# Optimization experiments

Hardware: AMD Instinct MI355X
Metric: run time of the kernel (lower is better)

## Reference

```python
import jax, jax.numpy as jnp
import numpy as np

NUM_POINTS = 4_000_000
RADIUS = 2.5
IMG = 1024


def setup_inputs() -> dict:
    key = jax.random.key(0)
    k1, k2, k3, k4 = jax.random.split(key, 4)
    # Uniform sampling inside a sphere, mirroring the torch __init__
    phi = jax.random.uniform(k1, (NUM_POINTS,)) * 2 * np.pi
    costheta = jax.random.uniform(k2, (NUM_POINTS,)) * 2 - 1
    u = jax.random.uniform(k3, (NUM_POINTS,))
    theta = jnp.arccos(costheta)
    r = RADIUS * u ** (1.0 / 3.0)
    x = r * jnp.sin(theta) * jnp.cos(phi)
    y = r * jnp.sin(theta) * jnp.sin(phi)
    z = r * jnp.cos(theta)
    positions = jnp.stack([x, y, z], axis=-1).astype(jnp.float32)  # [N,3]
    colors = jax.random.uniform(k4, (NUM_POINTS, 3), dtype=jnp.float32)
    # Camera at origin looking down +z, points translated to z in [2.5, 7.5]
    camera_pose = jnp.eye(4, dtype=jnp.float32).at[2, 3].set(5.0)
    intrinsics = jnp.array([[800.0, 0.0, 512.0],
                            [0.0, 800.0, 512.0],
                            [0.0, 0.0, 1.0]], dtype=jnp.float32)
    return {"positions": positions, "colors": colors,
            "camera_pose": camera_pose, "intrinsics": intrinsics,
            "H": IMG, "W": IMG}


def reference(positions, colors, camera_pose, intrinsics, H, W):
    # points_cam = (R @ P^T)^T + t^T
    R = camera_pose[:3, :3]
    t = camera_pose[:3, 3]
    pc = positions @ R.T + t  # [N,3]
    x, y, z = pc[:, 0], pc[:, 1], pc[:, 2]
    fx, fy = intrinsics[0, 0], intrinsics[1, 1]
    cx, cy = intrinsics[0, 2], intrinsics[1, 2]
    u = fx * x / z + cx
    v = fy * y / z + cy
    # int() truncation toward zero, matching the torch loop
    xi = u.astype(jnp.int32)
    yi = v.astype(jnp.int32)
    valid = (xi >= 0) & (xi < W) & (yi >= 0) & (yi < H)
    n = positions.shape[0]
    pix = jnp.where(valid, yi * W + xi, H * W)  # invalid -> sentinel segment
    winner = jax.ops.segment_max(jnp.arange(n, dtype=jnp.int32), pix,
                                 num_segments=H * W + 1)[: H * W]
    has = winner >= 0  # empty segments get iinfo(int32).min
    img_flat = jnp.where(has[:, None],
                         colors[jnp.clip(winner, 0, n - 1)],
                         jnp.float32(0.0))  # [H*W, 3]
    img = img_flat.reshape(H, W, 3).transpose(2, 0, 1)[None]  # [1,3,H,W]
    return jnp.clip(img, 0.0, 1.0)
```

## Files before the change

kernel.cpp:

```cpp
#include <hip/hip_runtime.h>


#define NB      1024
#define TB      512
#define NT      1024
#define PPB_MAX 4096
#define IMGW    1024
#define IMGHW   (1024 * 1024)

__host__ __device__ __forceinline__ unsigned align8u(unsigned x) {
    return (x + 7u) & ~7u;
}

__global__ void __launch_bounds__(TB)
binsort_kernel(const float* __restrict__ pos,
               const float* __restrict__ pose,
               const float* __restrict__ intr,
               unsigned* __restrict__ bins,
               unsigned* __restrict__ histG,
               int n, int ppb, int region) {
    __shared__ unsigned stash[PPB_MAX];
    __shared__ unsigned h[NT];
    __shared__ unsigned base_[NT];
    __shared__ unsigned cur[NT];
    __shared__ unsigned sc[TB];

    int tid = threadIdx.x;
    for (int t = tid; t < NT; t += TB) h[t] = 0;
    __syncthreads();

    float r00 = pose[0], r01 = pose[1], r02 = pose[2],  t0 = pose[3];
    float r10 = pose[4], r11 = pose[5], r12 = pose[6],  t1 = pose[7];
    float r20 = pose[8], r21 = pose[9], r22 = pose[10], t2 = pose[11];
    float fx = intr[0], cx = intr[2];
    float fy = intr[4], cy = intr[5];

    int start = blockIdx.x * ppb;
    int cnt = min(start + ppb, n) - start;
    if (cnt < 0) cnt = 0;

    const float4* p4 = (const float4*)(pos + (size_t)3 * (size_t)start);
    for (int j4 = tid * 4; j4 < cnt; j4 += TB * 4) {
        int g = j4 >> 2;
        float4 A = p4[3 * g + 0];
        float4 B = p4[3 * g + 1];
        float4 C = p4[3 * g + 2];
        float xs0 = A.x, ys0 = A.y, zs0 = A.z;
        float xs1 = A.w, ys1 = B.x, zs1 = B.y;
        float xs2 = B.z, ys2 = B.w, zs2 = C.x;
        float xs3 = C.y, ys3 = C.z, zs3 = C.w;

        unsigned pv[4];
        #define PROJ(K, PX, PY, PZ)                                          \
        {                                                                    \
            float x = r00 * PX + r01 * PY + r02 * PZ + t0;                   \
            float y = r10 * PX + r11 * PY + r12 * PZ + t1;                   \
            float z = r20 * PX + r21 * PY + r22 * PZ + t2;                   \
            float u = fx * x / z + cx;                                       \
            float v = fy * y / z + cy;                                       \
            int xi = (int)u;                                                 \
            int yi = (int)v;                                                 \
            unsigned p = 0xFFFFFFFFu;                                        \
            if (xi >= 0 && xi < IMGW && yi >= 0 && yi < IMGW) {              \
                p = ((unsigned)yi << 10) | (unsigned)xi;                     \
                int tt = ((yi >> 5) << 5) + (xi >> 5);                       \
                atomicAdd(&h[tt], 1u);                                       \
            }                                                                \
            pv[K] = p;                                                       \
        }
        PROJ(0, xs0, ys0, zs0)
        PROJ(1, xs1, ys1, zs1)
        PROJ(2, xs2, ys2, zs2)
        PROJ(3, xs3, ys3, zs3)
        #undef PROJ

        *(uint4*)&stash[j4] = make_uint4(pv[0], pv[1], pv[2], pv[3]);
    }
    __syncthreads();

    unsigned a0 = align8u(h[2 * tid]);
    unsigned a1 = align8u(h[2 * tid + 1]);
    unsigned v = a0 + a1;
    sc[tid] = v;
    __syncthreads();
    for (int off = 1; off < TB; off <<= 1) {
        unsigned add = (tid >= off) ? sc[tid - off] : 0u;
        __syncthreads();
        v += add;
        sc[tid] = v;
        __syncthreads();
    }
    base_[2 * tid]     = v - a0 - a1;
    base_[2 * tid + 1] = v - a1;
    __syncthreads();

    for (int t = tid; t < NT; t += TB) {
        cur[t] = base_[t];
        histG[(size_t)t * NB + blockIdx.x] = (base_[t] << 16) | h[t];
    }
    __syncthreads();

    unsigned* myRegion = bins + (size_t)blockIdx.x * (size_t)region;
    for (int j = tid; j < cnt; j += TB) {
        unsigned pv = stash[j];
        if (pv == 0xFFFFFFFFu) continue;
        unsigned xi = pv & 1023u, yi = pv >> 10;
        unsigned t  = ((yi >> 5) << 5) + (xi >> 5);
        unsigned lp = ((yi & 31u) << 5) + (xi & 31u);
        unsigned slot = atomicAdd(&cur[t], 1u);
        myRegion[slot] = (lp << 22) | (unsigned)(start + j);
    }
}

__global__ void __launch_bounds__(TB)
paint_kernel(const unsigned* __restrict__ bins,
             const unsigned* __restrict__ histG,
             const float* __restrict__ colors,
             float* __restrict__ out,
             int region) {
    __shared__ unsigned win[NT];
    int t = blockIdx.x;
    int tid = threadIdx.x;
    win[tid] = 0;
    win[tid + TB] = 0;
    __syncthreads();

    for (int b = tid; b < NB; b += TB) {
        unsigned pk = histG[(size_t)t * NB + b];
        unsigned sbase = pk >> 16, cnt = pk & 0xFFFFu;
        const unsigned* seg = bins + (size_t)b * (size_t)region + sbase;
        for (unsigned k = 0; k < cnt; ++k) {
            unsigned e = seg[k];
            atomicMax(&win[e >> 22], (e & 0x3FFFFFu) + 1u);
        }
    }
    __syncthreads();

    int tx = (t & 31) << 5, ty = (t >> 5) << 5;
    for (int l = tid; l < NT; l += TB) {
        unsigned w = win[l];
        float r = 0.0f, g = 0.0f, bl = 0.0f;
        if (w) {
            unsigned wi = w - 1u;
            r  = fminf(fmaxf(colors[3 * wi + 0], 0.0f), 1.0f);
            g  = fminf(fmaxf(colors[3 * wi + 1], 0.0f), 1.0f);
            bl = fminf(fmaxf(colors[3 * wi + 2], 0.0f), 1.0f);
        }
        int x = tx + (l & 31), y = ty + (l >> 5);
        int p = y * IMGW + x;
        out[p] = r;
        out[IMGHW + p] = g;
        out[2 * IMGHW + p] = bl;
    }
}


__global__ void proj_simple(const float* __restrict__ pos,
                            const float* __restrict__ pose,
                            const float* __restrict__ intr,
                            const int* __restrict__ Hp,
                            const int* __restrict__ Wp,
                            int* __restrict__ winner, int n) {
    int i = blockIdx.x * blockDim.x + threadIdx.x;
    if (i >= n) return;
    float px = pos[3 * i], py = pos[3 * i + 1], pz = pos[3 * i + 2];
    float x = pose[0] * px + pose[1] * py + pose[2]  * pz + pose[3];
    float y = pose[4] * px + pose[5] * py + pose[6]  * pz + pose[7];
    float z = pose[8] * px + pose[9] * py + pose[10] * pz + pose[11];
    float u = intr[0] * x / z + intr[2];
    float v = intr[4] * y / z + intr[5];
    int xi = (int)u, yi = (int)v;
    int W = *Wp, H = *Hp;
    if (xi >= 0 && xi < W && yi >= 0 && yi < H) atomicMax(&winner[yi * W + xi], i);
}

__global__ void paint_simple(const int* __restrict__ winner,
                             const float* __restrict__ colors,
                             float* __restrict__ out, int HW) {
    int p = blockIdx.x * blockDim.x + threadIdx.x;
    if (p >= HW) return;
    int w = winner[p];
    float r = 0.0f, g = 0.0f, b = 0.0f;
    if (w >= 0) {
        r = fminf(fmaxf(colors[3 * w + 0], 0.0f), 1.0f);
        g = fminf(fmaxf(colors[3 * w + 1], 0.0f), 1.0f);
        b = fminf(fmaxf(colors[3 * w + 2], 0.0f), 1.0f);
    }
    out[p] = r; out[HW + p] = g; out[2 * HW + p] = b;
}

extern "C" void kernel_launch(void* const* d_in, const int* in_sizes, int n_in,
                              void* d_out, int out_size, void* d_ws, size_t ws_size,
                              hipStream_t stream) {
    const float* positions = (const float*)d_in[0];
    const float* colors    = (const float*)d_in[1];
    const float* pose      = (const float*)d_in[2];
    const float* intr      = (const float*)d_in[3];
    const int*   Hp        = (const int*)d_in[4];
    const int*   Wp        = (const int*)d_in[5];
    float* out = (float*)d_out;

    int n  = in_sizes[0] / 3;
    int HW = out_size / 3;

    int ppb = ((n + NB - 1) / NB + 3) & ~3;
    int region = (int)align8u((unsigned)ppb) + 7 * NT;
    unsigned* bins  = (unsigned*)d_ws;
    unsigned* histG = bins + (size_t)NB * (size_t)region;
    size_t needFast = ((size_t)NB * region + (size_t)NT * NB) * sizeof(unsigned);

    bool fast = (HW == IMGHW) && (n >= 4096) && ((n & 3) == 0) &&
                (ppb <= PPB_MAX) && (n <= 4000000) && (ws_size >= needFast);

    if (fast) {
        binsort_kernel<<<NB, TB, 0, stream>>>(positions, pose, intr,
                                              bins, histG, n, ppb, region);
        paint_kernel<<<NT, TB, 0, stream>>>(bins, histG, colors, out, region);
        return;
    }

    int* winner = (int*)d_ws;
    const int block = 256;
    hipMemsetAsync(winner, 0xFF, (size_t)HW * sizeof(int), stream);
    int grid = (n + block - 1) / block;
    proj_simple<<<grid, block, 0, stream>>>(positions, pose, intr, Hp, Wp,
                                            winner, n);
    int grid2 = (HW + block - 1) / block;
    paint_simple<<<grid2, block, 0, stream>>>(winner, colors, out, HW);
}
```

Before: 71.16 us.

## Replace per-block bin regions with global tile-contiguous counting sort

Splits the fused bin-sort into histogram, two-level scan, and scatter kernels so that all points for a screen tile land contiguously in one global array. The paint kernel then walks one contiguous range per tile with all threads in parallel, instead of each thread serially reading many small per-block segments. In exchange it adds three extra kernel launches and a round trip of the per-point pixel codes through global memory rather than shared memory.

```diff
diff --git a/kernel.cpp b/kernel.cpp
--- a/kernel.cpp
+++ b/kernel.cpp
@@ -1,30 +1,20 @@
 #include <hip/hip_runtime.h>
 
 
-#define NB      1024
-#define TB      512
-#define NT      1024
-#define PPB_MAX 4096
-#define IMGW    1024
-#define IMGHW   (1024 * 1024)
-
-__host__ __device__ __forceinline__ unsigned align8u(unsigned x) {
-    return (x + 7u) & ~7u;
-}
+#define NB    1024
+#define TB    512
+#define NT    1024
+#define IMGW  1024
+#define IMGHW (1024 * 1024)
 
 __global__ void __launch_bounds__(TB)
-binsort_kernel(const float* __restrict__ pos,
-               const float* __restrict__ pose,
-               const float* __restrict__ intr,
-               unsigned* __restrict__ bins,
-               unsigned* __restrict__ histG,
-               int n, int ppb, int region) {
-    __shared__ unsigned stash[PPB_MAX];
+hist_kernel(const float* __restrict__ pos,
+            const float* __restrict__ pose,
+            const float* __restrict__ intr,
+            unsigned* __restrict__ pixArr,
+            unsigned* __restrict__ histB,
+            int n, int ppb) {
     __shared__ unsigned h[NT];
-    __shared__ unsigned base_[NT];
-    __shared__ unsigned cur[NT];
-    __shared__ unsigned sc[TB];
-
     int tid = threadIdx.x;
     for (int t = tid; t < NT; t += TB) h[t] = 0;
     __syncthreads();
@@ -40,6 +30,7 @@
     if (cnt < 0) cnt = 0;
 
     const float4* p4 = (const float4*)(pos + (size_t)3 * (size_t)start);
+    uint4* pa4 = (uint4*)(pixArr + start);
     for (int j4 = tid * 4; j4 < cnt; j4 += TB * 4) {
         int g = j4 >> 2;
         float4 A = p4[3 * g + 0];
@@ -58,7 +49,7 @@
             float z = r20 * PX + r21 * PY + r22 * PZ + t2;                   \
             float u = fx * x / z + cx;                                       \
             float v = fy * y / z + cy;                                       \
-            int xi = (int)u;                                                 \
+            int xi = (int)u;               \
             int yi = (int)v;                                                 \
             unsigned p = 0xFFFFFFFFu;                                        \
             if (xi >= 0 && xi < IMGW && yi >= 0 && yi < IMGW) {              \
@@ -74,70 +65,123 @@
         PROJ(3, xs3, ys3, zs3)
         #undef PROJ
 
-        *(uint4*)&stash[j4] = make_uint4(pv[0], pv[1], pv[2], pv[3]);
-    }
-    __syncthreads();
-
-    unsigned a0 = align8u(h[2 * tid]);
-    unsigned a1 = align8u(h[2 * tid + 1]);
-    unsigned v = a0 + a1;
+        pa4[g] = make_uint4(pv[0], pv[1], pv[2], pv[3]);
+    }
+    __syncthreads();
+
+    unsigned* hb = histB + (size_t)blockIdx.x * NT;
+    for (int t = tid; t < NT; t += TB) hb[t] = h[t];
+}
+
+__global__ void __launch_bounds__(256)
+scanA_kernel(const unsigned* __restrict__ histB,
+             unsigned* __restrict__ prefT,
+             unsigned* __restrict__ total) {
+    __shared__ unsigned sc[256];
+    int t = blockIdx.x;
+    int tid = threadIdx.x;
+
+    unsigned c0 = histB[(size_t)(4 * tid + 0) * NT + t];
+    unsigned c1 = histB[(size_t)(4 * tid + 1) * NT + t];
+    unsigned c2 = histB[(size_t)(4 * tid + 2) * NT + t];
+    unsigned c3 = histB[(size_t)(4 * tid + 3) * NT + t];
+    unsigned s = c0 + c1 + c2 + c3;
+
+    unsigned v = s;
     sc[tid] = v;
     __syncthreads();
-    for (int off = 1; off < TB; off <<= 1) {
+    for (int off = 1; off < 256; off <<= 1) {
         unsigned add = (tid >= off) ? sc[tid - off] : 0u;
         __syncthreads();
         v += add;
         sc[tid] = v;
         __syncthreads();
     }
-    base_[2 * tid]     = v - a0 - a1;
-    base_[2 * tid + 1] = v - a1;
-    __syncthreads();
-
-    for (int t = tid; t < NT; t += TB) {
-        cur[t] = base_[t];
-        histG[(size_t)t * NB + blockIdx.x] = (base_[t] << 16) | h[t];
-    }
-    __syncthreads();
-
-    unsigned* myRegion = bins + (size_t)blockIdx.x * (size_t)region;
-    for (int j = tid; j < cnt; j += TB) {
-        unsigned pv = stash[j];
-        if (pv == 0xFFFFFFFFu) continue;
-        unsigned xi = pv & 1023u, yi = pv >> 10;
-        unsigned t  = ((yi >> 5) << 5) + (xi >> 5);
-        unsigned lp = ((yi & 31u) << 5) + (xi & 31u);
-        unsigned slot = atomicAdd(&cur[t], 1u);
-        myRegion[slot] = (lp << 22) | (unsigned)(start + j);
-    }
+    unsigned excl = v - s;
+
+    unsigned* pt = prefT + (size_t)t * NB + 4 * tid;
+    pt[0] = excl;
+    pt[1] = excl + c0;
+    pt[2] = excl + c0 + c1;
+    pt[3] = excl + c0 + c1 + c2;
+    if (tid == 255) total[t] = v;
+}
+
+__global__ void __launch_bounds__(NT)
+scanB_kernel(const unsigned* __restrict__ total,
+             unsigned* __restrict__ tileBase) {
+    __shared__ unsigned sc[NT];
+    int t = threadIdx.x;
+    unsigned x = total[t];
+    unsigned v = x;
+    sc[t] = v;
+    __syncthreads();
+    for (int off = 1; off < NT; off <<= 1) {
+        unsigned add = (t >= off) ? sc[t - off] : 0u;
+        __syncthreads();
+        v += add;
+        sc[t] = v;
+        __syncthreads();
+    }
+    tileBase[t] = v - x;
+    if (t == NT - 1) tileBase[NT] = v;
 }
 
 __global__ void __launch_bounds__(TB)
-paint_kernel(const unsigned* __restrict__ bins,
-             const unsigned* __restrict__ histG,
+scatter_kernel(const unsigned* __restrict__ pixArr,
+               const unsigned* __restrict__ prefT,
+               const unsigned* __restrict__ tileBase,
+               unsigned* __restrict__ binsT,
+               int n, int ppb) {
+    __shared__ unsigned cur[NT];
+    int tid = threadIdx.x;
+    int b = blockIdx.x;
+    for (int t = tid; t < NT; t += TB)
+        cur[t] = tileBase[t] + prefT[(size_t)t * NB + b];
+    __syncthreads();
+
+    int start = b * ppb;
+    int cnt = min(start + ppb, n) - start;
+    if (cnt < 0) cnt = 0;
+
+    const uint4* pa4 = (const uint4*)(pixArr + start);
+    for (int j4 = tid * 4; j4 < cnt; j4 += TB * 4) {
+        uint4 q = pa4[j4 >> 2];
+        unsigned pvs[4] = {q.x, q.y, q.z, q.w};
+        #pragma unroll
+        for (int k = 0; k < 4; ++k) {
+            unsigned pv = pvs[k];
+            if (pv == 0xFFFFFFFFu) continue;
+            unsigned xi = pv & 1023u, yi = pv >> 10;
+            unsigned t  = ((yi >> 5) << 5) + (xi >> 5);
+            unsigned lp = ((yi & 31u) << 5) + (xi & 31u);
+            unsigned slot = atomicAdd(&cur[t], 1u);
+            binsT[slot] = (lp << 22) | (unsigned)(start + j4 + k);
+        }
+    }
+}
+
+__global__ void __launch_bounds__(256)
+paint_kernel(const unsigned* __restrict__ binsT,
+             const unsigned* __restrict__ tileBase,
              const float* __restrict__ colors,
-             float* __restrict__ out,
-             int region) {
+             float* __restrict__ out) {
     __shared__ unsigned win[NT];
     int t = blockIdx.x;
     int tid = threadIdx.x;
-    win[tid] = 0;
-    win[tid + TB] = 0;
-    __syncthreads();
-
-    for (int b = tid; b < NB; b += TB) {
-        unsigned pk = histG[(size_t)t * NB + b];
-        unsigned sbase = pk >> 16, cnt = pk & 0xFFFFu;
-        const unsigned* seg = bins + (size_t)b * (size_t)region + sbase;
-        for (unsigned k = 0; k < cnt; ++k) {
-            unsigned e = seg[k];
-            atomicMax(&win[e >> 22], (e & 0x3FFFFFu) + 1u);
-        }
+    #pragma unroll
+    for (int l = tid; l < NT; l += 256) win[l] = 0;
+    __syncthreads();
+
+    unsigned s0 = tileBase[t], s1 = tileBase[t + 1];
+    for (unsigned k = s0 + tid; k < s1; k += 256) {
+        unsigned e = binsT[k];
+        atomicMax(&win[e >> 22], (e & 0x3FFFFFu) + 1u);
     }
     __syncthreads();
 
     int tx = (t & 31) << 5, ty = (t >> 5) << 5;
-    for (int l = tid; l < NT; l += TB) {
+    for (int l = tid; l < NT; l += 256) {
         unsigned w = win[l];
         float r = 0.0f, g = 0.0f, bl = 0.0f;
         if (w) {
@@ -204,18 +248,27 @@
     int HW = out_size / 3;
 
     int ppb = ((n + NB - 1) / NB + 3) & ~3;
-    int region = (int)align8u((unsigned)ppb) + 7 * NT;
-    unsigned* bins  = (unsigned*)d_ws;
-    unsigned* histG = bins + (size_t)NB * (size_t)region;
-    size_t needFast = ((size_t)NB * region + (size_t)NT * NB) * sizeof(unsigned);
+
+    unsigned* pixArr   = (unsigned*)d_ws;
+    unsigned* binsT    = pixArr + n;
+    unsigned* histB    = binsT + n;
+    unsigned* prefT    = histB + (size_t)NB * NT;
+    unsigned* total    = prefT + (size_t)NT * NB;
+    unsigned* tileBase = total + NT;
+    size_t needFast = ((size_t)2 * n + 2 * (size_t)NB * NT + 2 * NT + 1)
+                      * sizeof(unsigned);
 
     bool fast = (HW == IMGHW) && (n >= 4096) && ((n & 3) == 0) &&
-                (ppb <= PPB_MAX) && (n <= 4000000) && (ws_size >= needFast);
+                (n <= 4000000) && (ws_size >= needFast);
 
     if (fast) {
-        binsort_kernel<<<NB, TB, 0, stream>>>(positions, pose, intr,
-                                              bins, histG, n, ppb, region);
-        paint_kernel<<<NT, TB, 0, stream>>>(bins, histG, colors, out, region);
+        hist_kernel<<<NB, TB, 0, stream>>>(positions, pose, intr,
+                                           pixArr, histB, n, ppb);
+        scanA_kernel<<<NT, 256, 0, stream>>>(histB, prefT, total);
+        scanB_kernel<<<1, NT, 0, stream>>>(total, tileBase);
+        scatter_kernel<<<NB, TB, 0, stream>>>(pixArr, prefT, tileBase,
+                                              binsT, n, ppb);
+        paint_kernel<<<NT, 256, 0, stream>>>(binsT, tileBase, colors, out);
         return;
     }
 
```

Result: slower. 83.53 us (+17.4%).
